# Optimization experiments

Hardware: AMD Instinct MI355X
Metric: run time of the kernel (lower is better)

Reference implementation:

```python
import jax, jax.numpy as jnp
import numpy as np

EPS = 1e-6

def setup_inputs() -> dict:
    key = jax.random.key(0)
    k1, k2, k3 = jax.random.split(key, 3)
    B, D, T = 4096, 4096, 16
    inputs = jax.random.normal(k1, (B, D), dtype=jnp.float32)
    W = jax.random.normal(k2, (D, T), dtype=jnp.float32)
    W_static = jax.random.normal(k3, (D, T), dtype=jnp.float32)
    return {"inputs": inputs, "W": W, "W_static": W_static}


def _znorm(A):
    # batch z-normalization per column (population std, matching tf.math.reduce_std)
    return (A - A.mean(axis=0)) / (A.std(axis=0) + EPS)


def _pls_scan(X, Ws):
    """Sequential PLS-style deflation: factor i is produced after
    orthogonalizing X against the z-normalized previous factors."""
    B = X.shape[0]
    denom = jnp.asarray(B, X.dtype)
    T = Ws.shape[1]
    cols = [X @ Ws[:, 0:1]]  # [B,1]
    for i in range(1, T):
        C = jnp.concatenate(cols, axis=1)          # [B,i]
        conv = _znorm(C)                           # [B,i]
        beta = (conv.T @ X) / denom                # [i,D]
        lin = X - conv @ beta                      # deflated inputs [B,D]
        cols.append(lin @ Ws[:, i:i + 1])
    return jnp.concatenate(cols, axis=1)           # [B,T]


def reference(inputs, W, W_static):
    # training path of FactorLayer.call
    X = _znorm(inputs)                              # batchnorm of inputs [B,D]
    c_mat = _pls_scan(X, W_static)                  # calculate_cmat with static weights
    B = X.shape[0]
    denom = jnp.asarray(B, X.dtype)
    T = W.shape[1]
    outs = [X @ W[:, 0:1]]
    for i in range(1, T):
        Cs = c_mat[:, :i]
        conv = _znorm(Cs)
        beta = (conv.T @ X) / denom                 # [i,D]
        lin = X - conv @ beta                       # training_run output [B,D]
        outs.append(lin @ W[:, i:i + 1])
    return jnp.concatenate(outs, axis=1)            # [B,T]
```

## Files before the change

### kernel.cpp

```cpp
#include <hip/hip_runtime.h>
#include <stdint.h>


#define BB 4096
#define DD 4096
#define EPSF 1e-6f

#define O_PART    0u
#define O_GRAMM   131072u
#define O_CNT     140032u
#define O_YPART   271360u

__device__ __forceinline__ int gidx(int a, int b) {
    int lo = a < b ? a : b, hi = a < b ? b : a;
    return lo * 33 + hi;
}

__device__ __forceinline__ float agl(const float* p) {
    unsigned int u = __hip_atomic_load((const unsigned int*)p,
                                       __ATOMIC_RELAXED, __HIP_MEMORY_SCOPE_AGENT);
    return __uint_as_float(u);
}

__global__ __launch_bounds__(256, 2)
void kA(const float* __restrict__ in, float* __restrict__ ws) {
    __shared__ float rs[8 * 132], rq[8 * 132];
    int b = blockIdx.x, t = threadIdx.x;
    int idx = b * 256 + t;
    if (idx < 8961) ws[O_GRAMM + idx] = 0.f;
    int cg = b & 31, rg = b >> 5;
    int dbase = cg * 128, r0 = rg * 256;
    int chunk = t & 31, rr = t >> 5;
    int c0 = dbase + chunk * 4;
    float s0=0.f,s1=0.f,s2=0.f,s3=0.f,q0=0.f,q1=0.f,q2=0.f,q3=0.f;
    #pragma unroll 4
    for (int i = 0; i < 32; ++i) {
        int r = r0 + i * 8 + rr;
        float4 u = *(const float4*)&in[(size_t)r * DD + c0];
        s0 += u.x; q0 += u.x*u.x;  s1 += u.y; q1 += u.y*u.y;
        s2 += u.z; q2 += u.z*u.z;  s3 += u.w; q3 += u.w*u.w;
    }
    int lb = rr * 132 + chunk * 4;
    rs[lb+0]=s0; rs[lb+1]=s1; rs[lb+2]=s2; rs[lb+3]=s3;
    rq[lb+0]=q0; rq[lb+1]=q1; rq[lb+2]=q2; rq[lb+3]=q3;
    __syncthreads();
    float* part = ws + O_PART + (size_t)rg * 8192;
    if (t < 128) {
        float a = 0.f;
        #pragma unroll
        for (int r2 = 0; r2 < 8; ++r2) a += rs[r2 * 132 + t];
        part[dbase + t] = a;
    } else {
        int ci = t - 128;
        float a = 0.f;
        #pragma unroll
        for (int r2 = 0; r2 < 8; ++r2) a += rq[r2 * 132 + ci];
        part[4096 + dbase + ci] = a;
    }
}

__global__ __launch_bounds__(256, 8)
void kB(const float* __restrict__ in, const float* __restrict__ W,
        const float* __restrict__ Wstat, float* __restrict__ ws,
        float* __restrict__ ypart) {
    __shared__ __align__(16) float tile[64 * 33];
    __shared__ __align__(16) float inv_s[128];
    int b = blockIdx.x, t = threadIdx.x;
    int dg = b & 31, rg = b >> 5;
    int dbase = dg * 128, rowbase = rg * 64;
    int chunk = t & 7, srow = t >> 3;
    int row = t & 63;
    int jq = __builtin_amdgcn_readfirstlane(t >> 6);
    const float* inp = in + (size_t)(rowbase + srow) * DD + dbase + chunk * 4;
    float4 pf0 = *(const float4*)(inp);
    float4 pf1 = *(const float4*)(inp + (size_t)32 * DD);
    {
        if (t < 128) {
            const float* part = ws + O_PART;
            float s = 0.f, q = 0.f;
            #pragma unroll
            for (int g = 0; g < 16; ++g) {
                s += part[(size_t)g * 8192 + dbase + t];
                q += part[(size_t)g * 8192 + 4096 + dbase + t];
            }
            float m = s * (1.0f / BB);
            float var = q * (1.0f / BB) - m * m; if (var < 0.f) var = 0.f;
            inv_s[t] = 1.0f / (sqrtf(var) + EPSF);
        }
        __syncthreads();
    }
    float acc[8];
    #pragma unroll
    for (int i = 0; i < 8; ++i) acc[i] = 0.f;
    const float* wbase = (jq < 2) ? (Wstat + jq * 8) : (W + (jq - 2) * 8);
    for (int stage = 0; stage < 4; ++stage) {
        int ds0 = stage * 32;
        float4 iv4 = *(const float4*)&inv_s[ds0 + chunk * 4];
        int b0 = srow * 33 + chunk * 4;
        tile[b0 + 0] = pf0.x * iv4.x; tile[b0 + 1] = pf0.y * iv4.y;
        tile[b0 + 2] = pf0.z * iv4.z; tile[b0 + 3] = pf0.w * iv4.w;
        int b1 = (srow + 32) * 33 + chunk * 4;
        tile[b1 + 0] = pf1.x * iv4.x; tile[b1 + 1] = pf1.y * iv4.y;
        tile[b1 + 2] = pf1.z * iv4.z; tile[b1 + 3] = pf1.w * iv4.w;
        __syncthreads();
        if (stage < 3) {
            pf0 = *(const float4*)(inp + (stage + 1) * 32);
            pf1 = *(const float4*)(inp + (size_t)32 * DD + (stage + 1) * 32);
        }
        const float* trow = tile + row * 33;
        #pragma unroll 4
        for (int dl = 0; dl < 32; ++dl) {
            float xs = trow[dl];
            const float* wr = wbase + (size_t)(dbase + ds0 + dl) * 16;
            #pragma unroll
            for (int j = 0; j < 8; ++j) acc[j] += xs * wr[j];
        }
        __syncthreads();
    }
    float* dst = ypart + ((size_t)dg * BB + rowbase + row) * 32 + jq * 8;
    *(float4*)(dst + 0) = make_float4(acc[0], acc[1], acc[2], acc[3]);
    *(float4*)(dst + 4) = make_float4(acc[4], acc[5], acc[6], acc[7]);
}

__global__ __launch_bounds__(512, 1)
void kCE(float* __restrict__ ws, float* __restrict__ out) {
    __shared__ __align__(16) float yzs[64 * 36];
    __shared__ float Sv[33], GA[17 * 17], gz[17 * 16], v[15][17], gad[15][16],
                     gzd[15][16], gu[17], u[17], st[2], wm[17 * 16];
    int b = blockIdx.x, t = threadIdx.x;
    int rowbase = b * 64;
    const float invB = 1.0f / BB;

    {
        int r = t >> 3, q = (t & 7) * 4;
        const float* yp = ws + O_YPART;
        size_t off = (size_t)(rowbase + r) * 32 + q;
        float x0=0.f, x1=0.f, x2=0.f, x3=0.f;
        #pragma unroll 8
        for (int dg = 0; dg < 32; ++dg) {
            float4 vv = *(const float4*)&yp[(size_t)dg * (BB * 32) + off];
            x0 += vv.x; x1 += vv.y; x2 += vv.z; x3 += vv.w;
        }
        int lb = r * 36 + q;
        yzs[lb + 0] = x0; yzs[lb + 1] = x1; yzs[lb + 2] = x2; yzs[lb + 3] = x3;
        if (q == 0) yzs[r * 36 + 32] = 1.0f;
    }
    __syncthreads();

    float* gm8 = ws + O_GRAMM + (size_t)(b & 7) * 1120;
    for (int p = t; p < 561; p += 512) {
        int i = 0, rem = p;
        while (rem >= 33 - i) { rem -= 33 - i; ++i; }
        int j = i + rem;
        float a2 = 0.f;
        #pragma unroll 8
        for (int r2 = 0; r2 < 64; ++r2)
            a2 += yzs[r2 * 36 + i] * yzs[r2 * 36 + j];
        atomicAdd(&gm8[i * 33 + j], a2);
    }

    __syncthreads();
    unsigned int* cnt = (unsigned int*)(ws + O_CNT);
    if (t == 0) {
        atomicAdd(cnt, 1u);
        while (__hip_atomic_load(cnt, __ATOMIC_RELAXED,
                                 __HIP_MEMORY_SCOPE_AGENT) < 64u)
            __builtin_amdgcn_s_sleep(8);
    }
    __syncthreads();

    const float* gm = ws + O_GRAMM;
    if (t < 33) {
        float s = 0.f;
        #pragma unroll
        for (int m = 0; m < 8; ++m) s += agl(&gm[m * 1120 + gidx(t, 32)]);
        Sv[t] = s;
    }
    __syncthreads();
    for (int idx = t; idx < 17 * 17; idx += 512) {
        int p = idx / 17, q = idx % 17;
        float val;
        if (p < 16 && q < 16) {
            float raw = 0.f;
            #pragma unroll
            for (int m = 0; m < 8; ++m) raw += agl(&gm[m * 1120 + gidx(p, q)]);
            val = raw - Sv[p] * Sv[q] * invB;
        } else if (p == 16 && q == 16) val = (float)BB;
        else val = 0.f;
        GA[idx] = val;
    }
    for (int idx = t; idx < 17 * 16; idx += 512) {
        int p = idx / 16, tt = idx % 16;
        float val = 0.f;
        if (p < 16) {
            float raw = 0.f;
            #pragma unroll
            for (int m = 0; m < 8; ++m) raw += agl(&gm[m * 1120 + gidx(p, 16 + tt)]);
            val = raw - Sv[p] * Sv[16 + tt] * invB;
        }
        gz[idx] = val;
    }
    if (t < 17) u[t] = (t == 0) ? 1.f : 0.f;
    __syncthreads();
    for (int i = 0; i < 15; ++i) {
        if (t < 17) {
            float s = 0.f;
            for (int q = 0; q < 17; ++q) s += GA[t * 17 + q] * u[q];
            gu[t] = s;
        }
        __syncthreads();
        if (t == 0) {
            float mean = gu[16] * invB, e2 = 0.f;
            for (int p = 0; p < 17; ++p) e2 += u[p] * gu[p];
            e2 *= invB;
            float var = e2 - mean * mean; if (var < 0.f) var = 0.f;
            st[0] = mean; st[1] = 1.0f / (sqrtf(var) + EPSF);
        }
        __syncthreads();
        if (t < 17) v[i][t] = (u[t] - (t == 16 ? st[0] : 0.f)) * st[1];
        __syncthreads();
        if (t < 16) {
            float s = 0.f;
            for (int p = 0; p < 17; ++p) s += v[i][p] * GA[p * 17 + t];
            gad[i][t] = s;
        } else if (t < 32) {
            int tt = t - 16;
            float s = 0.f;
            for (int p = 0; p < 17; ++p) s += v[i][p] * gz[p * 16 + tt];
            gzd[i][tt] = s;
        }
        __syncthreads();
        if (t < 17) {
            float a2 = 0.f;
            for (int j = 0; j <= i; ++j) a2 += v[j][t] * gad[j][i + 1];
            u[t] = ((t == i + 1) ? 1.f : 0.f) - a2 * invB;
        }
        __syncthreads();
    }
    for (int idx = t; idx < 17 * 16; idx += 512) {
        int p = idx / 16, tt = idx % 16;
        float s = 0.f;
        for (int j = 0; j < tt; ++j) s += v[j][p] * gzd[j][tt];
        wm[idx] = s * invB;
    }
    __syncthreads();
    if (t < 16) {
        float adj = Sv[16 + t] * invB;
        for (int p = 0; p < 16; ++p) adj -= Sv[p] * invB * wm[p * 16 + t];
        wm[16 * 16 + t] += adj;
    }
    __syncthreads();
    if (t < 256) {
        int row = t >> 2, c0 = (t & 3) * 4;
        const float* yr = yzs + row * 36;
        float o[4];
        #pragma unroll
        for (int k = 0; k < 4; ++k) o[k] = yr[16 + c0 + k] - wm[16 * 16 + c0 + k];
        #pragma unroll
        for (int p = 0; p < 16; ++p) {
            float yp = yr[p];
            #pragma unroll
            for (int k = 0; k < 4; ++k) o[k] -= yp * wm[p * 16 + c0 + k];
        }
        *(float4*)&out[(size_t)rowbase * 16 + t * 4] = make_float4(o[0], o[1], o[2], o[3]);
    }
}

extern "C" void kernel_launch(void* const* d_in, const int* in_sizes, int n_in,
                              void* d_out, int out_size, void* d_ws, size_t ws_size,
                              hipStream_t stream) {
    const float* in    = (const float*)d_in[0];
    const float* W     = (const float*)d_in[1];
    const float* Wstat = (const float*)d_in[2];
    float* ws  = (float*)d_ws;
    float* out = (float*)d_out;

    kA<<<dim3(512),  dim3(256), 0, stream>>>(in, ws);
    kB<<<dim3(2048), dim3(256), 0, stream>>>(in, W, Wstat, ws, ws + O_YPART);
    kCE<<<dim3(64),  dim3(512), 0, stream>>>(ws, out);
}
```

Baseline: 146.8 us.

## Fuse column-stats pass into projection kernel with per-column-group spin barrier

Removes the separate statistics kernel. Each projection block now loads its whole 64x128 input tile into registers, reduces column sums and sums of squares in shared memory, and adds them atomically into global accumulators. It then spins on a per-column-group counter until all 64 row blocks have contributed, and reuses the register-held tile for the scaled projection. This is meant to read the input from memory once instead of twice. The cost is global atomics, a software grid barrier that depends on all blocks being resident at once (risk of deadlock), higher register pressure, and a memset of the workspace.

```diff
diff --git a/kernel.cpp b/kernel.cpp
--- a/kernel.cpp
+++ b/kernel.cpp
@@ -6,10 +6,13 @@
 #define DD 4096
 #define EPSF 1e-6f
 
-#define O_PART    0u
-#define O_GRAMM   131072u
-#define O_CNT     140032u
-#define O_YPART   271360u
+#define O_SUM     0u
+#define O_SQ      4096u
+#define O_GRAMM   8192u
+#define O_CNTDG   17152u
+#define O_CNTF    17184u
+#define ZERO_BYTES (17185u * 4u)
+#define O_YPART   17408u
 
 __device__ __forceinline__ int gidx(int a, int b) {
     int lo = a < b ? a : b, hi = a < b ? b : a;
@@ -22,47 +25,10 @@
     return __uint_as_float(u);
 }
 
-__global__ __launch_bounds__(256, 2)
-void kA(const float* __restrict__ in, float* __restrict__ ws) {
-    __shared__ float rs[8 * 132], rq[8 * 132];
-    int b = blockIdx.x, t = threadIdx.x;
-    int idx = b * 256 + t;
-    if (idx < 8961) ws[O_GRAMM + idx] = 0.f;
-    int cg = b & 31, rg = b >> 5;
-    int dbase = cg * 128, r0 = rg * 256;
-    int chunk = t & 31, rr = t >> 5;
-    int c0 = dbase + chunk * 4;
-    float s0=0.f,s1=0.f,s2=0.f,s3=0.f,q0=0.f,q1=0.f,q2=0.f,q3=0.f;
-    #pragma unroll 4
-    for (int i = 0; i < 32; ++i) {
-        int r = r0 + i * 8 + rr;
-        float4 u = *(const float4*)&in[(size_t)r * DD + c0];
-        s0 += u.x; q0 += u.x*u.x;  s1 += u.y; q1 += u.y*u.y;
-        s2 += u.z; q2 += u.z*u.z;  s3 += u.w; q3 += u.w*u.w;
-    }
-    int lb = rr * 132 + chunk * 4;
-    rs[lb+0]=s0; rs[lb+1]=s1; rs[lb+2]=s2; rs[lb+3]=s3;
-    rq[lb+0]=q0; rq[lb+1]=q1; rq[lb+2]=q2; rq[lb+3]=q3;
-    __syncthreads();
-    float* part = ws + O_PART + (size_t)rg * 8192;
-    if (t < 128) {
-        float a = 0.f;
-        #pragma unroll
-        for (int r2 = 0; r2 < 8; ++r2) a += rs[r2 * 132 + t];
-        part[dbase + t] = a;
-    } else {
-        int ci = t - 128;
-        float a = 0.f;
-        #pragma unroll
-        for (int r2 = 0; r2 < 8; ++r2) a += rq[r2 * 132 + ci];
-        part[4096 + dbase + ci] = a;
-    }
-}
-
 __global__ __launch_bounds__(256, 8)
-void kB(const float* __restrict__ in, const float* __restrict__ W,
-        const float* __restrict__ Wstat, float* __restrict__ ws,
-        float* __restrict__ ypart) {
+void kAB(const float* __restrict__ in, const float* __restrict__ W,
+         const float* __restrict__ Wstat, float* __restrict__ ws,
+         float* __restrict__ ypart) {
     __shared__ __align__(16) float tile[64 * 33];
     __shared__ __align__(16) float inv_s[128];
     int b = blockIdx.x, t = threadIdx.x;
@@ -72,23 +38,54 @@
     int row = t & 63;
     int jq = __builtin_amdgcn_readfirstlane(t >> 6);
     const float* inp = in + (size_t)(rowbase + srow) * DD + dbase + chunk * 4;
-    float4 pf0 = *(const float4*)(inp);
-    float4 pf1 = *(const float4*)(inp + (size_t)32 * DD);
-    {
-        if (t < 128) {
-            const float* part = ws + O_PART;
-            float s = 0.f, q = 0.f;
-            #pragma unroll
-            for (int g = 0; g < 16; ++g) {
-                s += part[(size_t)g * 8192 + dbase + t];
-                q += part[(size_t)g * 8192 + 4096 + dbase + t];
-            }
-            float m = s * (1.0f / BB);
-            float var = q * (1.0f / BB) - m * m; if (var < 0.f) var = 0.f;
-            inv_s[t] = 1.0f / (sqrtf(var) + EPSF);
-        }
-        __syncthreads();
-    }
+
+    float4 f0[4], f1[4];
+    #pragma unroll
+    for (int s = 0; s < 4; ++s) {
+        f0[s] = *(const float4*)(inp + s * 32);
+        f1[s] = *(const float4*)(inp + (size_t)32 * DD + s * 32);
+    }
+
+    float* sbuf = tile;
+    float* qbuf = tile + 1056;
+    for (int s = 0; s < 4; ++s) {
+        float4 a = f0[s], c = f1[s];
+        int lb = srow * 33 + chunk * 4;
+        sbuf[lb+0] = a.x + c.x; qbuf[lb+0] = a.x*a.x + c.x*c.x;
+        sbuf[lb+1] = a.y + c.y; qbuf[lb+1] = a.y*a.y + c.y*c.y;
+        sbuf[lb+2] = a.z + c.z; qbuf[lb+2] = a.z*a.z + c.z*c.z;
+        sbuf[lb+3] = a.w + c.w; qbuf[lb+3] = a.w*a.w + c.w*c.w;
+        __syncthreads();
+        if (t < 64) {
+            int col = t & 31;
+            const float* bufp = (t >= 32) ? qbuf : sbuf;
+            float acc = 0.f;
+            #pragma unroll
+            for (int r = 0; r < 32; ++r) acc += bufp[r * 33 + col];
+            unsigned int base = (t >= 32) ? O_SQ : O_SUM;
+            atomicAdd(&ws[base + dbase + s * 32 + col], acc);
+        }
+        __syncthreads();
+    }
+
+    unsigned int* cdg = (unsigned int*)(ws + O_CNTDG);
+    if (t == 0) {
+        atomicAdd(&cdg[dg], 1u);
+        while (__hip_atomic_load(&cdg[dg], __ATOMIC_RELAXED,
+                                 __HIP_MEMORY_SCOPE_AGENT) < 64u)
+            __builtin_amdgcn_s_sleep(2);
+    }
+    __syncthreads();
+
+    if (t < 128) {
+        float s = agl(&ws[O_SUM + dbase + t]);
+        float q = agl(&ws[O_SQ + dbase + t]);
+        float m = s * (1.0f / BB);
+        float var = q * (1.0f / BB) - m * m; if (var < 0.f) var = 0.f;
+        inv_s[t] = 1.0f / (sqrtf(var) + EPSF);
+    }
+    __syncthreads();
+
     float acc[8];
     #pragma unroll
     for (int i = 0; i < 8; ++i) acc[i] = 0.f;
@@ -96,17 +93,14 @@
     for (int stage = 0; stage < 4; ++stage) {
         int ds0 = stage * 32;
         float4 iv4 = *(const float4*)&inv_s[ds0 + chunk * 4];
+        float4 a = f0[stage], c = f1[stage];
         int b0 = srow * 33 + chunk * 4;
-        tile[b0 + 0] = pf0.x * iv4.x; tile[b0 + 1] = pf0.y * iv4.y;
-        tile[b0 + 2] = pf0.z * iv4.z; tile[b0 + 3] = pf0.w * iv4.w;
+        tile[b0 + 0] = a.x * iv4.x; tile[b0 + 1] = a.y * iv4.y;
+        tile[b0 + 2] = a.z * iv4.z; tile[b0 + 3] = a.w * iv4.w;
         int b1 = (srow + 32) * 33 + chunk * 4;
-        tile[b1 + 0] = pf1.x * iv4.x; tile[b1 + 1] = pf1.y * iv4.y;
-        tile[b1 + 2] = pf1.z * iv4.z; tile[b1 + 3] = pf1.w * iv4.w;
-        __syncthreads();
-        if (stage < 3) {
-            pf0 = *(const float4*)(inp + (stage + 1) * 32);
-            pf1 = *(const float4*)(inp + (size_t)32 * DD + (stage + 1) * 32);
-        }
+        tile[b1 + 0] = c.x * iv4.x; tile[b1 + 1] = c.y * iv4.y;
+        tile[b1 + 2] = c.z * iv4.z; tile[b1 + 3] = c.w * iv4.w;
+        __syncthreads();
         const float* trow = tile + row * 33;
         #pragma unroll 4
         for (int dl = 0; dl < 32; ++dl) {
@@ -160,7 +154,7 @@
     }
 
     __syncthreads();
-    unsigned int* cnt = (unsigned int*)(ws + O_CNT);
+    unsigned int* cnt = (unsigned int*)(ws + O_CNTF);
     if (t == 0) {
         atomicAdd(cnt, 1u);
         while (__hip_atomic_load(cnt, __ATOMIC_RELAXED,
@@ -275,7 +269,7 @@
     float* ws  = (float*)d_ws;
     float* out = (float*)d_out;
 
-    kA<<<dim3(512),  dim3(256), 0, stream>>>(in, ws);
-    kB<<<dim3(2048), dim3(256), 0, stream>>>(in, W, Wstat, ws, ws + O_YPART);
-    kCE<<<dim3(64),  dim3(512), 0, stream>>>(ws, out);
-}
+    hipMemsetAsync(ws, 0, ZERO_BYTES, stream);
+    kAB<<<dim3(2048), dim3(256), 0, stream>>>(in, W, Wstat, ws, ws + O_YPART);
+    kCE<<<dim3(64),   dim3(512), 0, stream>>>(ws, out);
+}
```

Result: slower. 255.3 us (+73.9%).

## Fuse final reduction kernel into GEMV kernel via last-block-per-rowgroup election

Applied to the files above, without the earlier changes.

Merges the kCE epilogue into kB. The last of the 32 column blocks to finish each row group, found with an atomic counter, performs the y-partial reduction, Gram accumulation, grid barrier and small solve. Partial stores and loads become agent-scope atomics so the elected block sees the other blocks' data. This removes one kernel launch and the tail gap between kernels. In exchange, the epilogue now runs with 256 threads instead of 512, and the cross-block spin barrier relies on all 64 elected blocks being resident at the same time.

```diff
diff --git a/kernel.cpp b/kernel.cpp
--- a/kernel.cpp
+++ b/kernel.cpp
@@ -8,8 +8,9 @@
 
 #define O_PART    0u
 #define O_GRAMM   131072u
-#define O_CNT     140032u
-#define O_YPART   271360u
+#define O_CNTRG   140032u
+#define O_CNTF    140096u
+#define O_YPART   140288u
 
 __device__ __forceinline__ int gidx(int a, int b) {
     int lo = a < b ? a : b, hi = a < b ? b : a;
@@ -20,6 +21,20 @@
     unsigned int u = __hip_atomic_load((const unsigned int*)p,
                                        __ATOMIC_RELAXED, __HIP_MEMORY_SCOPE_AGENT);
     return __uint_as_float(u);
+}
+
+__device__ __forceinline__ void ast2(float* p, float a, float b) {
+    unsigned long long u = (unsigned long long)__float_as_uint(a)
+                         | ((unsigned long long)__float_as_uint(b) << 32);
+    __hip_atomic_store((unsigned long long*)p, u,
+                       __ATOMIC_RELAXED, __HIP_MEMORY_SCOPE_AGENT);
+}
+
+__device__ __forceinline__ void ald2(const float* p, float& a, float& b) {
+    unsigned long long u = __hip_atomic_load((const unsigned long long*)p,
+                                             __ATOMIC_RELAXED, __HIP_MEMORY_SCOPE_AGENT);
+    a = __uint_as_float((unsigned int)u);
+    b = __uint_as_float((unsigned int)(u >> 32));
 }
 
 __global__ __launch_bounds__(256, 2)
@@ -27,7 +42,7 @@
     __shared__ float rs[8 * 132], rq[8 * 132];
     int b = blockIdx.x, t = threadIdx.x;
     int idx = b * 256 + t;
-    if (idx < 8961) ws[O_GRAMM + idx] = 0.f;
+    if (idx < 9216) ws[O_GRAMM + idx] = 0.f;
     int cg = b & 31, rg = b >> 5;
     int dbase = cg * 128, r0 = rg * 256;
     int chunk = t & 31, rr = t >> 5;
@@ -60,11 +75,13 @@
 }
 
 __global__ __launch_bounds__(256, 8)
-void kB(const float* __restrict__ in, const float* __restrict__ W,
-        const float* __restrict__ Wstat, float* __restrict__ ws,
-        float* __restrict__ ypart) {
-    __shared__ __align__(16) float tile[64 * 33];
-    __shared__ __align__(16) float inv_s[128];
+void kBCE(const float* __restrict__ in, const float* __restrict__ W,
+          const float* __restrict__ Wstat, float* __restrict__ ws,
+          float* __restrict__ ypart, float* __restrict__ out) {
+    __shared__ __align__(16) float arena[3968];
+    __shared__ int s_last;
+    float* tile  = arena;
+    float* inv_s = arena + 2112;
     int b = blockIdx.x, t = threadIdx.x;
     int dg = b & 31, rg = b >> 5;
     int dbase = dg * 128, rowbase = rg * 64;
@@ -118,28 +135,43 @@
         __syncthreads();
     }
     float* dst = ypart + ((size_t)dg * BB + rowbase + row) * 32 + jq * 8;
-    *(float4*)(dst + 0) = make_float4(acc[0], acc[1], acc[2], acc[3]);
-    *(float4*)(dst + 4) = make_float4(acc[4], acc[5], acc[6], acc[7]);
-}
-
-__global__ __launch_bounds__(512, 1)
-void kCE(float* __restrict__ ws, float* __restrict__ out) {
-    __shared__ __align__(16) float yzs[64 * 36];
-    __shared__ float Sv[33], GA[17 * 17], gz[17 * 16], v[15][17], gad[15][16],
-                     gzd[15][16], gu[17], u[17], st[2], wm[17 * 16];
-    int b = blockIdx.x, t = threadIdx.x;
-    int rowbase = b * 64;
+    ast2(dst + 0, acc[0], acc[1]);
+    ast2(dst + 2, acc[2], acc[3]);
+    ast2(dst + 4, acc[4], acc[5]);
+    ast2(dst + 6, acc[6], acc[7]);
+
+    __syncthreads();
+    unsigned int* crg = (unsigned int*)(ws + O_CNTRG);
+    if (t == 0) s_last = (atomicAdd(&crg[rg], 1u) == 31u);
+    __syncthreads();
+    if (!s_last) return;
+
+    float* yzs = arena;
+    float* Sv  = arena + 2304;
+    float* GA  = arena + 2337;
+    float* gz  = arena + 2626;
+    float* vv_ = arena + 2898;
+    float* gad = arena + 3153;
+    float* gzd = arena + 3393;
+    float* gu  = arena + 3633;
+    float* u   = arena + 3650;
+    float* st  = arena + 3667;
+    float* wm  = arena + 3669;
     const float invB = 1.0f / BB;
 
-    {
-        int r = t >> 3, q = (t & 7) * 4;
-        const float* yp = ws + O_YPART;
+    #pragma unroll
+    for (int k = 0; k < 2; ++k) {
+        int idx = k * 256 + t;
+        int r = idx >> 3, q = (idx & 7) * 4;
         size_t off = (size_t)(rowbase + r) * 32 + q;
         float x0=0.f, x1=0.f, x2=0.f, x3=0.f;
         #pragma unroll 8
-        for (int dg = 0; dg < 32; ++dg) {
-            float4 vv = *(const float4*)&yp[(size_t)dg * (BB * 32) + off];
-            x0 += vv.x; x1 += vv.y; x2 += vv.z; x3 += vv.w;
+        for (int dg2 = 0; dg2 < 32; ++dg2) {
+            const float* p = &ypart[(size_t)dg2 * (BB * 32) + off];
+            float a0, a1, a2, a3;
+            ald2(p + 0, a0, a1);
+            ald2(p + 2, a2, a3);
+            x0 += a0; x1 += a1; x2 += a2; x3 += a3;
         }
         int lb = r * 36 + q;
         yzs[lb + 0] = x0; yzs[lb + 1] = x1; yzs[lb + 2] = x2; yzs[lb + 3] = x3;
@@ -147,8 +179,8 @@
     }
     __syncthreads();
 
-    float* gm8 = ws + O_GRAMM + (size_t)(b & 7) * 1120;
-    for (int p = t; p < 561; p += 512) {
+    float* gm8 = ws + O_GRAMM + (size_t)(rg & 7) * 1120;
+    for (int p = t; p < 561; p += 256) {
         int i = 0, rem = p;
         while (rem >= 33 - i) { rem -= 33 - i; ++i; }
         int j = i + rem;
@@ -160,7 +192,7 @@
     }
 
     __syncthreads();
-    unsigned int* cnt = (unsigned int*)(ws + O_CNT);
+    unsigned int* cnt = (unsigned int*)(ws + O_CNTF);
     if (t == 0) {
         atomicAdd(cnt, 1u);
         while (__hip_atomic_load(cnt, __ATOMIC_RELAXED,
@@ -177,7 +209,7 @@
         Sv[t] = s;
     }
     __syncthreads();
-    for (int idx = t; idx < 17 * 17; idx += 512) {
+    for (int idx = t; idx < 17 * 17; idx += 256) {
         int p = idx / 17, q = idx % 17;
         float val;
         if (p < 16 && q < 16) {
@@ -189,7 +221,7 @@
         else val = 0.f;
         GA[idx] = val;
     }
-    for (int idx = t; idx < 17 * 16; idx += 512) {
+    for (int idx = t; idx < 17 * 16; idx += 256) {
         int p = idx / 16, tt = idx % 16;
         float val = 0.f;
         if (p < 16) {
@@ -217,30 +249,30 @@
             st[0] = mean; st[1] = 1.0f / (sqrtf(var) + EPSF);
         }
         __syncthreads();
-        if (t < 17) v[i][t] = (u[t] - (t == 16 ? st[0] : 0.f)) * st[1];
+        if (t < 17) vv_[i * 17 + t] = (u[t] - (t == 16 ? st[0] : 0.f)) * st[1];
         __syncthreads();
         if (t < 16) {
             float s = 0.f;
-            for (int p = 0; p < 17; ++p) s += v[i][p] * GA[p * 17 + t];
-            gad[i][t] = s;
+            for (int p = 0; p < 17; ++p) s += vv_[i * 17 + p] * GA[p * 17 + t];
+            gad[i * 16 + t] = s;
         } else if (t < 32) {
             int tt = t - 16;
             float s = 0.f;
-            for (int p = 0; p < 17; ++p) s += v[i][p] * gz[p * 16 + tt];
-            gzd[i][tt] = s;
+            for (int p = 0; p < 17; ++p) s += vv_[i * 17 + p] * gz[p * 16 + tt];
+            gzd[i * 16 + tt] = s;
         }
         __syncthreads();
         if (t < 17) {
             float a2 = 0.f;
-            for (int j = 0; j <= i; ++j) a2 += v[j][t] * gad[j][i + 1];
+            for (int j = 0; j <= i; ++j) a2 += vv_[j * 17 + t] * gad[j * 16 + i + 1];
             u[t] = ((t == i + 1) ? 1.f : 0.f) - a2 * invB;
         }
         __syncthreads();
     }
-    for (int idx = t; idx < 17 * 16; idx += 512) {
+    for (int idx = t; idx < 17 * 16; idx += 256) {
         int p = idx / 16, tt = idx % 16;
         float s = 0.f;
-        for (int j = 0; j < tt; ++j) s += v[j][p] * gzd[j][tt];
+        for (int j = 0; j < tt; ++j) s += vv_[j * 17 + p] * gzd[j * 16 + tt];
         wm[idx] = s * invB;
     }
     __syncthreads();
@@ -250,9 +282,9 @@
         wm[16 * 16 + t] += adj;
     }
     __syncthreads();
-    if (t < 256) {
-        int row = t >> 2, c0 = (t & 3) * 4;
-        const float* yr = yzs + row * 36;
+    {
+        int r = t >> 2, c0 = (t & 3) * 4;
+        const float* yr = yzs + r * 36;
         float o[4];
         #pragma unroll
         for (int k = 0; k < 4; ++k) o[k] = yr[16 + c0 + k] - wm[16 * 16 + c0 + k];
@@ -275,7 +307,6 @@
     float* ws  = (float*)d_ws;
     float* out = (float*)d_out;
 
-    kA<<<dim3(512),  dim3(256), 0, stream>>>(in, ws);
-    kB<<<dim3(2048), dim3(256), 0, stream>>>(in, W, Wstat, ws, ws + O_YPART);
-    kCE<<<dim3(64),  dim3(512), 0, stream>>>(ws, out);
-}
+    kA<<<dim3(512),   dim3(256), 0, stream>>>(in, ws);
+    kBCE<<<dim3(2048), dim3(256), 0, stream>>>(in, W, Wstat, ws, ws + O_YPART, out);
+}
```

Result: slower. 204.2 us (+39.1%).
